# Performance work log

Measured on AMD Instinct MI355X. Metric: run time of the kernel, lower is better.

Reference implementation:

```python
import jax, jax.numpy as jnp
import numpy as np
import math

B = 8192          # per_replica_batch_size
D = 256           # embedding_dim
R = 8             # num_relations
N = 1024          # in_batch_negatives
F = 2             # embedding features per node (summed)


def setup_inputs() -> dict:
    key = jax.random.key(0)
    k_emb, k_tr = jax.random.split(key)
    emb = jax.random.normal(k_emb, (2 * B, F, D), dtype=jnp.float32)
    trans_embs = jax.random.uniform(k_tr, (R, D), dtype=jnp.float32)
    # relations: equal count per relation so shapes are static under jit
    rels_np = (np.arange(B) % R).astype(np.int32)
    order_np = np.argsort(rels_np, kind='stable').astype(np.int32)  # rows grouped by relation
    rng = np.random.default_rng(0)
    C = B // R
    reps = math.ceil(N / C)
    neg_lhs = np.empty((R, N), dtype=np.int32)
    neg_rhs = np.empty((R, N), dtype=np.int32)
    for r in range(R):  # small fixed loop over relations, host-side only
        rows = np.where(rels_np == r)[0]
        neg_lhs[r] = rows[np.tile(rng.permutation(C), reps)[:N]]
        neg_rhs[r] = rows[np.tile(rng.permutation(C), reps)[:N]]
    return {
        'emb': emb,
        'trans_embs': trans_embs,
        'rels': jnp.asarray(rels_np),
        'order': jnp.asarray(order_np),
        'neg_lhs_idx': jnp.asarray(neg_lhs),
        'neg_rhs_idx': jnp.asarray(neg_rhs),
    }


def reference(emb, trans_embs, rels, order, neg_lhs_idx, neg_rhs_idx):
    b = rels.shape[0]
    d = emb.shape[-1]
    r, n = neg_lhs_idx.shape
    c = b // r
    # sum feature embeddings per node, split into (lhs, rhs) pairs
    x = jnp.sum(emb, axis=1).reshape(b, 2, d)
    lhs = x[:, 0, :]
    rhs = x[:, 1, :]
    translated = rhs + trans_embs[rels]
    pos = jnp.sum(lhs * translated, axis=-1)  # [B]
    # relation-grouped rows (stable original order within each relation)
    s_lhs = lhs[order].reshape(r, c, d)
    s_rhs = rhs[order].reshape(r, c, d)
    samp_lhs = lhs[neg_lhs_idx]  # [R, N, D]
    samp_rhs = rhs[neg_rhs_idx]  # [R, N, D]
    # negs_lhs = rhs_matrix @ sampled_lhs.T ; negs_rhs = lhs_matrix @ sampled_rhs.T
    negs_lhs = jnp.einsum('rcd,rnd->rcn', s_rhs, samp_lhs).reshape(r, c * n)
    negs_rhs = jnp.einsum('rcd,rnd->rcn', s_lhs, samp_rhs).reshape(r, c * n)
    # per relation: [negs_lhs_flat, negs_rhs_flat], concatenated over relations
    negs = jnp.concatenate([negs_lhs, negs_rhs], axis=1).reshape(-1)
    logits = jnp.concatenate([pos, negs])
    return logits, jax.nn.sigmoid(logits)
```

## Files before the change

### kernel.cpp

```cpp
#include <hip/hip_runtime.h>
#include <hip/hip_bf16.h>
#include <stdint.h>

#define B_SZ 8192
#define D_SZ 256
#define R_SZ 8
#define N_SZ 1024
#define C_SZ (B_SZ / R_SZ)
#define CN   (C_SZ * N_SZ)
#define L_SZ (B_SZ + 2 * R_SZ * CN)

#define FP_SCALE 1792.0f
#define FP_INV_S2 3.113918e-7f

typedef int   i32x4 __attribute__((ext_vector_type(4)));
typedef float f32x4 __attribute__((ext_vector_type(4)));

static __device__ __forceinline__ float sigmoidf_(float x) {
  return 1.0f / (1.0f + __expf(-x));
}
static __device__ __forceinline__ void gload16(const void* g, void* l) {
  __builtin_amdgcn_global_load_lds(
      (const __attribute__((address_space(1))) void*)g,
      (__attribute__((address_space(3))) void*)l, 16, 0, 0);
}


__global__ __launch_bounds__(256) void prep_kernel(
    const float* __restrict__ emb, const float* __restrict__ trans,
    const int* __restrict__ rels, float* __restrict__ out,
    char* __restrict__ ws) {
  char* lhs_H = ws;
  char* lhs_L = ws + ((size_t)2 << 20);
  char* rhs_H = ws + ((size_t)4 << 20);
  char* rhs_L = ws + ((size_t)6 << 20);

  int wave = threadIdx.x >> 6;
  int lane = threadIdx.x & 63;
  int i = blockIdx.x * 4 + wave;

  const float4* emb4 = (const float4*)emb;
  size_t bl = (size_t)(2 * i) * 128;
  size_t br = (size_t)(2 * i + 1) * 128;
  float4 a0 = emb4[bl + lane];
  float4 a1 = emb4[bl + 64 + lane];
  float4 b0 = emb4[br + lane];
  float4 b1 = emb4[br + 64 + lane];
  float lh[4] = {a0.x + a1.x, a0.y + a1.y, a0.z + a1.z, a0.w + a1.w};
  float rh[4] = {b0.x + b1.x, b0.y + b1.y, b0.z + b1.z, b0.w + b1.w};

  int rel = rels[i];
  float4 tv = ((const float4*)trans)[rel * 64 + lane];
  float tt[4] = {tv.x, tv.y, tv.z, tv.w};

  float p = 0.f;
#pragma unroll
  for (int j = 0; j < 4; ++j) p += lh[j] * (rh[j] + tt[j]);
#pragma unroll
  for (int off = 32; off; off >>= 1) p += __shfl_xor(p, off, 64);
  if (lane == 0) {
    out[i] = p;
    out[(size_t)L_SZ + i] = sigmoidf_(p);
  }

  int phL = 0, plL = 0, phR = 0, plR = 0;
#pragma unroll
  for (int j = 0; j < 4; ++j) {
    float t = fminf(fmaxf(lh[j] * FP_SCALE, -16256.f), 16256.f);
    int hi = __float2int_rn(t * 0.0078125f);
    int lo = __float2int_rn(t) - (hi << 7);
    phL |= (hi & 255) << (8 * j);
    plL |= (lo & 255) << (8 * j);
    t = fminf(fmaxf(rh[j] * FP_SCALE, -16256.f), 16256.f);
    hi = __float2int_rn(t * 0.0078125f);
    lo = __float2int_rn(t) - (hi << 7);
    phR |= (hi & 255) << (8 * j);
    plR |= (lo & 255) << (8 * j);
  }
  size_t rowb = (size_t)i * 256 + lane * 4;
  *(int*)(lhs_H + rowb) = phL;
  *(int*)(lhs_L + rowb) = plL;
  *(int*)(rhs_H + rowb) = phR;
  *(int*)(rhs_L + rowb) = plR;
}

__global__ __launch_bounds__(256, 2) void negs_kernel(
    const char* __restrict__ ws,
    const int* __restrict__ order,
    const int* __restrict__ negL, const int* __restrict__ negR,
    float* __restrict__ out) {
  __shared__ char lds[2][4][8192];

  const char* lhs_H = ws;
  const char* lhs_L = ws + ((size_t)2 << 20);
  const char* rhs_H = ws + ((size_t)4 << 20);
  const char* rhs_L = ws + ((size_t)6 << 20);

  int bid = blockIdx.x;
  int ntile = bid & 7;
  int ctile = (bid >> 3) & 7;
  int side  = (bid >> 6) & 1;
  int r     = bid >> 7;

  int wave = threadIdx.x >> 6;
  int lane = threadIdx.x & 63;
  int wrow = wave >> 1, wcol = wave & 1;
  int lx = lane & 15;

  const char* srcp;
  const int* idxp;
  int idxbase;
  if (wave < 2) {
    idxp = order;
    idxbase = r * C_SZ + ctile * 128;
    srcp = (wave == 0) ? (side ? lhs_H : rhs_H) : (side ? lhs_L : rhs_L);
  } else {
    idxp = side ? negR : negL;
    idxbase = r * N_SZ + ntile * 128;
    srcp = (wave == 2) ? (side ? rhs_H : lhs_H) : (side ? rhs_L : lhs_L);
  }

  unsigned srcswz = (unsigned)(((lane & 3) ^ ((lane >> 3) & 3)) << 4);
  unsigned goff[8];
#pragma unroll
  for (int it = 0; it < 8; ++it) {
    int grow = idxp[idxbase + it * 16 + (lane >> 2)];
    goff[it] = (unsigned)grow * 256u + srcswz;
  }

  i32x4 acc1[4][4] = {};
  i32x4 acc2[4][4] = {};
  int q = lane >> 4;

#pragma unroll
  for (int it = 0; it < 8; ++it)
    gload16(srcp + goff[it], &lds[0][wave][0] + it * 1024);
  __syncthreads();

#pragma unroll 1
  for (int kc = 0; kc < 4; ++kc) {
    if (kc < 3) {
      char* nl = &lds[(kc + 1) & 1][wave][0];
#pragma unroll
      for (int it = 0; it < 8; ++it)
        gload16(srcp + goff[it] + (unsigned)(kc + 1) * 64u, nl + it * 1024);
    }

    const char* L0 = &lds[kc & 1][0][0];
    i32x4 ha[4], la[4], hb[4], lb[4];
#pragma unroll
    for (int mi = 0; mi < 4; ++mi) {
      int row = wrow * 64 + mi * 16 + lx;
      int off = row * 64 + ((q ^ ((row >> 1) & 3)) << 4);
      ha[mi] = *(const i32x4*)(L0 + off);
      la[mi] = *(const i32x4*)(L0 + 8192 + off);
    }
#pragma unroll
    for (int ni = 0; ni < 4; ++ni) {
      int row = wcol * 64 + ni * 16 + lx;
      int off = row * 64 + ((q ^ ((row >> 1) & 3)) << 4);
      hb[ni] = *(const i32x4*)(L0 + 16384 + off);
      lb[ni] = *(const i32x4*)(L0 + 24576 + off);
    }
#pragma unroll
    for (int mi = 0; mi < 4; ++mi)
#pragma unroll
      for (int ni = 0; ni < 4; ++ni) {
        acc1[mi][ni] = __builtin_amdgcn_mfma_i32_16x16x64_i8(ha[mi], hb[ni], acc1[mi][ni], 0, 0, 0);
        acc2[mi][ni] = __builtin_amdgcn_mfma_i32_16x16x64_i8(la[mi], hb[ni], acc2[mi][ni], 0, 0, 0);
        acc2[mi][ni] = __builtin_amdgcn_mfma_i32_16x16x64_i8(ha[mi], lb[ni], acc2[mi][ni], 0, 0, 0);
      }

    __syncthreads();
  }

  size_t obase = (size_t)B_SZ + ((size_t)(r * 2 + side)) * CN;
  int gcb = ntile * 128 + wcol * 64 + lx;
  int grb = ctile * 128 + wrow * 64 + ((lane >> 4) << 2);
#pragma unroll
  for (int mi = 0; mi < 4; ++mi) {
#pragma unroll
    for (int jj = 0; jj < 4; ++jj) {
      int gr = grb + mi * 16 + jj;
      size_t rowb = obase + (size_t)gr * N_SZ;
      float v[4], s[4];
#pragma unroll
      for (int ni = 0; ni < 4; ++ni) {
        v[ni] = fmaf(16384.0f, (float)acc1[mi][ni][jj],
                     128.0f * (float)acc2[mi][ni][jj]) * FP_INV_S2;
        s[ni] = sigmoidf_(v[ni]);
      }
#pragma unroll
      for (int ni = 0; ni < 4; ++ni)
        out[rowb + gcb + ni * 16] = v[ni];
#pragma unroll
      for (int ni = 0; ni < 4; ++ni)
        out[(size_t)L_SZ + rowb + gcb + ni * 16] = s[ni];
    }
  }
}

extern "C" void kernel_launch(void* const* d_in, const int* in_sizes, int n_in,
                              void* d_out, int out_size, void* d_ws, size_t ws_size,
                              hipStream_t stream) {
  const float* emb   = (const float*)d_in[0];
  const float* trans = (const float*)d_in[1];
  const int*   rels  = (const int*)d_in[2];
  const int*   order = (const int*)d_in[3];
  const int*   negL  = (const int*)d_in[4];
  const int*   negR  = (const int*)d_in[5];
  float* out = (float*)d_out;
  char* ws = (char*)d_ws;

  prep_kernel<<<B_SZ / 4, 256, 0, stream>>>(emb, trans, rels, out, ws);
  negs_kernel<<<R_SZ * 2 * 8 * 8, 256, 0, stream>>>(ws, order, negL, negR, out);
}
```

Measured before the change: 48.20 us.

## Load A operand directly from global into registers, halve LDS, remap block order

The A-side (order-gathered) hi/lo rows are now read straight from global memory into registers per wave, and only the B-side negatives are staged through LDS. This halves LDS use (32KB to 16KB) so the launch bound can ask for 3 blocks per CU. Block IDs are also permuted so that consecutive hardware blocks spread across relations and sides, which may change cache locality. The cost is that A loads now come from global memory with no LDS reuse and can stall the MFMA loop, since waves sharing a row tile load the same data twice.

```diff
diff --git a/kernel.cpp b/kernel.cpp
--- a/kernel.cpp
+++ b/kernel.cpp
@@ -84,19 +84,20 @@
   *(int*)(rhs_L + rowb) = plR;
 }
 
-__global__ __launch_bounds__(256, 2) void negs_kernel(
+__global__ __launch_bounds__(256, 3) void negs_kernel(
     const char* __restrict__ ws,
     const int* __restrict__ order,
     const int* __restrict__ negL, const int* __restrict__ negR,
     float* __restrict__ out) {
-  __shared__ char lds[2][4][8192];
+  __shared__ char lds[2][2][8192];
 
   const char* lhs_H = ws;
   const char* lhs_L = ws + ((size_t)2 << 20);
   const char* rhs_H = ws + ((size_t)4 << 20);
   const char* rhs_L = ws + ((size_t)6 << 20);
 
-  int bid = blockIdx.x;
+  int hw = blockIdx.x;
+  int bid = (hw & 7) * 128 + (hw >> 3);
   int ntile = bid & 7;
   int ctile = (bid >> 3) & 7;
   int side  = (bid >> 6) & 1;
@@ -106,26 +107,31 @@
   int lane = threadIdx.x & 63;
   int wrow = wave >> 1, wcol = wave & 1;
   int lx = lane & 15;
-
-  const char* srcp;
-  const int* idxp;
-  int idxbase;
-  if (wave < 2) {
-    idxp = order;
-    idxbase = r * C_SZ + ctile * 128;
-    srcp = (wave == 0) ? (side ? lhs_H : rhs_H) : (side ? lhs_L : rhs_L);
-  } else {
-    idxp = side ? negR : negL;
-    idxbase = r * N_SZ + ntile * 128;
-    srcp = (wave == 2) ? (side ? rhs_H : lhs_H) : (side ? rhs_L : lhs_L);
-  }
-
+  int kq = lane >> 4;
+
+  const char* aHi = side ? lhs_H : rhs_H;
+  const char* aLo = side ? lhs_L : rhs_L;
+  const char* bHi = side ? rhs_H : lhs_H;
+  const char* bLo = side ? rhs_L : lhs_L;
+  const int* negp = side ? negR : negL;
+
+  unsigned aoff[4];
+  {
+    int ab = r * C_SZ + ctile * 128 + wrow * 64 + lx;
+#pragma unroll
+    for (int mi = 0; mi < 4; ++mi)
+      aoff[mi] = (unsigned)order[ab + mi * 16] * 256u + (unsigned)kq * 16u;
+  }
+
+  int arr = wave >> 1, half = wave & 1;
+  const char* bsrc = arr ? bLo : bHi;
   unsigned srcswz = (unsigned)(((lane & 3) ^ ((lane >> 3) & 3)) << 4);
-  unsigned goff[8];
-#pragma unroll
-  for (int it = 0; it < 8; ++it) {
-    int grow = idxp[idxbase + it * 16 + (lane >> 2)];
-    goff[it] = (unsigned)grow * 256u + srcswz;
+  unsigned goff[4];
+  {
+    int nb = r * N_SZ + ntile * 128 + half * 64;
+#pragma unroll
+    for (int it = 0; it < 4; ++it)
+      goff[it] = (unsigned)negp[nb + it * 16 + (lane >> 2)] * 256u + srcswz;
   }
 
   i32x4 acc1[4][4] = {};
@@ -133,35 +139,36 @@
   int q = lane >> 4;
 
 #pragma unroll
-  for (int it = 0; it < 8; ++it)
-    gload16(srcp + goff[it], &lds[0][wave][0] + it * 1024);
+  for (int it = 0; it < 4; ++it)
+    gload16(bsrc + goff[it], &lds[0][arr][half * 4096] + it * 1024);
   __syncthreads();
 
 #pragma unroll 1
   for (int kc = 0; kc < 4; ++kc) {
     if (kc < 3) {
-      char* nl = &lds[(kc + 1) & 1][wave][0];
-#pragma unroll
-      for (int it = 0; it < 8; ++it)
-        gload16(srcp + goff[it] + (unsigned)(kc + 1) * 64u, nl + it * 1024);
+      char* nl = &lds[(kc + 1) & 1][arr][half * 4096];
+#pragma unroll
+      for (int it = 0; it < 4; ++it)
+        gload16(bsrc + goff[it] + (unsigned)(kc + 1) * 64u, nl + it * 1024);
+    }
+
+    i32x4 ha[4], la[4];
+#pragma unroll
+    for (int mi = 0; mi < 4; ++mi) {
+      ha[mi] = *(const i32x4*)(aHi + (aoff[mi] + (unsigned)kc * 64u));
+      la[mi] = *(const i32x4*)(aLo + (aoff[mi] + (unsigned)kc * 64u));
     }
 
     const char* L0 = &lds[kc & 1][0][0];
-    i32x4 ha[4], la[4], hb[4], lb[4];
-#pragma unroll
-    for (int mi = 0; mi < 4; ++mi) {
-      int row = wrow * 64 + mi * 16 + lx;
-      int off = row * 64 + ((q ^ ((row >> 1) & 3)) << 4);
-      ha[mi] = *(const i32x4*)(L0 + off);
-      la[mi] = *(const i32x4*)(L0 + 8192 + off);
-    }
+    i32x4 hb[4], lb[4];
 #pragma unroll
     for (int ni = 0; ni < 4; ++ni) {
       int row = wcol * 64 + ni * 16 + lx;
       int off = row * 64 + ((q ^ ((row >> 1) & 3)) << 4);
-      hb[ni] = *(const i32x4*)(L0 + 16384 + off);
-      lb[ni] = *(const i32x4*)(L0 + 24576 + off);
-    }
+      hb[ni] = *(const i32x4*)(L0 + off);
+      lb[ni] = *(const i32x4*)(L0 + 8192 + off);
+    }
+
 #pragma unroll
     for (int mi = 0; mi < 4; ++mi)
 #pragma unroll
```

New measurement: 63.74 us. 32.2% more time.
